# Optimization experiments

Hardware: AMD Instinct MI355X
Metric: run time of the kernel (lower is better)

## Reference

```python
import jax, jax.numpy as jnp
import numpy as np

HIDDEN_DIM = 128


def setup_inputs() -> dict:
    key = jax.random.key(0)
    ks = jax.random.split(key, 7)
    n_edges, edge_dim, edge_hidden, d = 20000, 16, 128, HIDDEN_DIM
    h_v = jax.random.normal(ks[0], (n_edges, d), dtype=jnp.float32)
    h_w = jax.random.normal(ks[1], (n_edges, d), dtype=jnp.float32)
    edge_features = jax.random.normal(ks[2], (n_edges, edge_dim), dtype=jnp.float32)
    W1 = jax.random.normal(ks[3], (edge_dim, edge_hidden), dtype=jnp.float32) * (1.0 / np.sqrt(edge_dim))
    b1 = jnp.zeros((edge_hidden,), dtype=jnp.float32)
    W2 = jax.random.normal(ks[4], (edge_hidden, d * d), dtype=jnp.float32) * (1.0 / np.sqrt(edge_hidden))
    b2 = jnp.zeros((d * d,), dtype=jnp.float32)
    return {"h_v": h_v, "h_w": h_w, "edge_features": edge_features,
            "W1": W1, "b1": b1, "W2": W2, "b2": b2}


def reference(h_v, h_w, edge_features, W1, b1, W2, b2):
    d = HIDDEN_DIM
    # Edge MLP: edge_dim -> edge_hidden -> d*d
    hidden = jax.nn.relu(edge_features @ W1 + b1)          # (E, edge_hidden)
    A = (hidden @ W2 + b2).reshape(-1, d, d)               # (E, d, d) per-edge matrices
    # Batched matrix-vector product: messages_e = A_e @ h_w_e
    messages = jnp.einsum('eij,ej->ei', A, h_w)            # (E, d)
    return messages
```

## Files before the change

kernel.cpp:

```cpp
#include <hip/hip_runtime.h>

#define E_EDGES 20000
#define D_DIM   128
#define NPAIRS  65
#define HSLICES 132

#define NBA 130
#define NBH 313
#define NBC 320

typedef __bf16 bf16x8 __attribute__((ext_vector_type(8)));
typedef float  floatx4 __attribute__((ext_vector_type(4)));

__device__ __forceinline__ unsigned short f32_to_bf16_rne(float f) {
    unsigned int u = __float_as_uint(f);
    unsigned int r = u + 0x7FFFu + ((u >> 16) & 1u);
    return (unsigned short)(r >> 16);
}

__device__ __forceinline__ void gload_lds16(const void* g, void* l) {
    __builtin_amdgcn_global_load_lds(
        (const __attribute__((address_space(1))) unsigned int*)g,
        (__attribute__((address_space(3))) unsigned int*)l, 16, 0, 0);
}

__global__ __launch_bounds__(256) void prep_all(
    const float* __restrict__ W2, const float* __restrict__ b2,
    const float* __restrict__ ef, const float* __restrict__ W1,
    const float* __restrict__ b1, const float* __restrict__ hw,
    uint4* __restrict__ bpf, unsigned int* __restrict__ hTp,
    unsigned short* __restrict__ hwb)
{
    __shared__ __align__(16) char pmem[34816];
    const int bx = blockIdx.x;
    const int t  = threadIdx.x;

    if (bx < NBA) {
        const int h = bx;
        if (h < 129) {
            unsigned short* tile = (unsigned short*)pmem;
            const float* src = (h < 128) ? (W2 + (size_t)h * (D_DIM * D_DIM)) : b2;
            #pragma unroll
            for (int r = 0; r < 16; ++r) {
                const float4 v = ((const float4*)src)[r * 256 + t];
                int c   = (r * 256 + t) * 4;
                int col = c >> 7;
                int k   = c & 127;
                unsigned int u0 = f32_to_bf16_rne(v.x) | ((unsigned int)f32_to_bf16_rne(v.y) << 16);
                unsigned int u1 = f32_to_bf16_rne(v.z) | ((unsigned int)f32_to_bf16_rne(v.w) << 16);
                *(uint2*)&tile[col * 136 + k] = make_uint2(u0, u1);
            }
            __syncthreads();
            #pragma unroll
            for (int r2 = 0; r2 < 8; ++r2) {
                int cidx = r2 * 256 + t;
                int g  = cidx >> 8;
                int s  = (cidx >> 6) & 3;
                int ll = cidx & 63;
                int col = 16 * g + (ll & 15);
                int k0  = 32 * s + 8 * (ll >> 4);
                bpf[(size_t)h * 2048 + cidx] = *(const uint4*)&tile[col * 136 + k0];
            }
        } else {
            #pragma unroll
            for (int r2 = 0; r2 < 8; ++r2)
                bpf[(size_t)h * 2048 + r2 * 256 + t] = make_uint4(0, 0, 0, 0);
        }
    } else if (bx < NBA + NBH) {
        float (*lds_ef)[17] = (float(*)[17])pmem;
        const int b  = bx - NBA;
        const int e0 = b * 64;
        {
            int e  = t >> 2;
            int k4 = (t & 3) * 4;
            int ge = e0 + e;
            float4 v = make_float4(0.f, 0.f, 0.f, 0.f);
            if (ge < E_EDGES) v = *(const float4*)(ef + (size_t)ge * 16 + k4);
            lds_ef[e][k4 + 0] = v.x; lds_ef[e][k4 + 1] = v.y;
            lds_ef[e][k4 + 2] = v.z; lds_ef[e][k4 + 3] = v.w;
        }
        __syncthreads();
        const int e  = t & 63;
        const int hg = t >> 6;
        const bool valid = (e0 + e) < E_EDGES;
        float efr[16];
        #pragma unroll
        for (int k = 0; k < 16; ++k) efr[k] = lds_ef[e][k];
        #pragma unroll 4
        for (int hi2 = 0; hi2 < 16; ++hi2) {
            int h0 = hg * 32 + 2 * hi2;
            float a0 = b1[h0], a1 = b1[h0 + 1];
            #pragma unroll
            for (int k = 0; k < 16; ++k) {
                a0 += efr[k] * W1[k * 128 + h0];
                a1 += efr[k] * W1[k * 128 + h0 + 1];
            }
            unsigned int pk = (unsigned int)f32_to_bf16_rne(fmaxf(a0, 0.f))
                            | ((unsigned int)f32_to_bf16_rne(fmaxf(a1, 0.f)) << 16);
            if (valid) hTp[(size_t)(hg * 16 + hi2) * E_EDGES + e0 + e] = pk;
        }
        if (hg == 0 && valid)
            hTp[(size_t)64 * E_EDGES + e0 + e] = 0x00003F80u;
    } else {
        int i0 = (bx - NBA - NBH) * 256 + t;
        for (int i = i0; i < (E_EDGES * D_DIM) / 4; i += NBC * 256) {
            const float4 v = ((const float4*)hw)[i];
            union { unsigned short u16[4]; uint2 u2; } o;
            o.u16[0] = f32_to_bf16_rne(v.x);
            o.u16[1] = f32_to_bf16_rne(v.y);
            o.u16[2] = f32_to_bf16_rne(v.z);
            o.u16[3] = f32_to_bf16_rne(v.w);
            ((uint2*)hwb)[i] = o.u2;
        }
    }
}

__global__ __launch_bounds__(512, 2)
void edge_main(const uint4* __restrict__ bpf, const unsigned int* __restrict__ hTp,
               const uint4* __restrict__ hwb, float* __restrict__ out) {
    __shared__ __align__(16) char smem[65536];
    const int bx  = blockIdx.x;
    const int ch  = bx & 1;
    const int eg  = bx >> 1;
    const int tid = threadIdx.x;
    const int w   = tid >> 6;
    const int l   = tid & 63;
    const int l4  = l >> 4;
    const int lm  = l & 15;
    const int g   = w & 3;
    const int eh  = w >> 2;
    const int e0  = eg * 160;
    const int eA  = e0 + eh * 80;

    bf16x8 A[5][4];
    #pragma unroll
    for (int m = 0; m < 5; ++m)
        #pragma unroll
        for (int s = 0; s < 4; ++s)
            A[m][s] = ((const bf16x8*)hwb)[(eA + 16 * m + lm) * 16 + 4 * s + l4];

    floatx4 C[5];
    #pragma unroll
    for (int m = 0; m < 5; ++m) C[m] = (floatx4){0.f, 0.f, 0.f, 0.f};
    const floatx4 Zf = (floatx4){0.f, 0.f, 0.f, 0.f};

    const char* bpf_c = (const char*)bpf;

    auto stage = [&](int pair, int p) {
        #pragma unroll
        for (int hh = 0; hh < 2; ++hh) {
            const int h = 2 * pair + hh;
            const char* src = bpf_c + ((size_t)(h * 8 + 4 * ch) * 256) * 16;
            char* dst = smem + p * 32768 + hh * 16384;
            #pragma unroll
            for (int r = 0; r < 2; ++r) {
                const int off = (r * 512 + w * 64) * 16;
                gload_lds16(src + off + l * 16, dst + off);
            }
        }
    };
    auto loadHP = [&](int pair, uint4 (&hp)[5]) {
        const unsigned int* row = hTp + (size_t)pair * E_EDGES + eA + 4 * l4;
        #pragma unroll
        for (int m = 0; m < 5; ++m) hp[m] = *(const uint4*)(row + 16 * m);
    };
    auto computeH = [&](int p, int hh, const uint4 (&hp)[5], bool odd) {
        const bf16x8* Bb = (const bf16x8*)(smem + p * 32768 + hh * 16384) + g * 256 + l;
        bf16x8 B[4];
        #pragma unroll
        for (int s = 0; s < 4; ++s) B[s] = Bb[s * 64];
        #pragma unroll
        for (int m = 0; m < 5; ++m) {
            floatx4 D = __builtin_amdgcn_mfma_f32_16x16x32_bf16(A[m][0], B[0], Zf, 0, 0, 0);
            #pragma unroll
            for (int s = 1; s < 4; ++s)
                D = __builtin_amdgcn_mfma_f32_16x16x32_bf16(A[m][s], B[s], D, 0, 0, 0);
            #pragma unroll
            for (int r = 0; r < 4; ++r) {
                unsigned int u = hp[m][r];
                float sc = odd ? __uint_as_float(u & 0xFFFF0000u)
                               : __uint_as_float(u << 16);
                C[m][r] += sc * D[r];
            }
        }
    };

    uint4 hpa[5], hpb[5];
    stage(0, 0);
    loadHP(0, hpa);
    for (int pr = 0; pr < 64; pr += 2) {
        __syncthreads();
        stage(pr + 1, 1);
        loadHP(pr + 1, hpb);
        computeH(0, 0, hpa, false);
        computeH(0, 1, hpa, true);
        __syncthreads();
        stage(pr + 2, 0);
        loadHP(pr + 2, hpa);
        computeH(1, 0, hpb, false);
        computeH(1, 1, hpb, true);
    }
    __syncthreads();
    computeH(0, 0, hpa, false);
    computeH(0, 1, hpa, true);

    #pragma unroll
    for (int m = 0; m < 5; ++m)
        #pragma unroll
        for (int r = 0; r < 4; ++r)
            out[(size_t)(eA + 16 * m + 4 * l4 + r) * D_DIM + 64 * ch + 16 * g + lm] = C[m][r];
}

extern "C" void kernel_launch(void* const* d_in, const int* in_sizes, int n_in,
                              void* d_out, int out_size, void* d_ws, size_t ws_size,
                              hipStream_t stream) {
    const float* h_w = (const float*)d_in[1];
    const float* ef  = (const float*)d_in[2];
    const float* W1  = (const float*)d_in[3];
    const float* b1  = (const float*)d_in[4];
    const float* W2  = (const float*)d_in[5];
    const float* b2  = (const float*)d_in[6];
    float* out = (float*)d_out;

    char* ws = (char*)d_ws;
    uint4*          bpf = (uint4*)ws;
    unsigned int*   hTp = (unsigned int*)(ws + 4325376);
    unsigned short* hwb = (unsigned short*)(ws + 4325376 + 5200000);

    hipLaunchKernelGGL(prep_all, dim3(NBA + NBH + NBC), dim3(256), 0, stream,
                       W2, b2, ef, W1, b1, h_w, bpf, hTp, hwb);
    hipLaunchKernelGGL(edge_main, dim3(250), dim3(512), 0, stream,
                       bpf, hTp, (const uint4*)hwb, out);
}
```

Measured before the change: 185.4 us.

## Split-K edge_main across two block halves with atomic accumulation into zeroed output

Splits the K (hidden-vector) dimension of the per-edge matvec across two blocks, so each block runs half the MFMAs per slice. Grid size roughly doubles, and the slices are processed four at a time per pipeline stage. Results are merged with atomicAdd into an output cleared by hipMemsetAsync, and launch bounds are raised to request more waves per SIMD. The bpf layout and slice padding (66 pairs) are reworked to match. In exchange it adds an extra memset, atomic traffic, and twice the hTp scale loads across blocks.

```diff
diff --git a/kernel.cpp b/kernel.cpp
--- a/kernel.cpp
+++ b/kernel.cpp
@@ -2,10 +2,10 @@
 
 #define E_EDGES 20000
 #define D_DIM   128
-#define NPAIRS  65
 #define HSLICES 132
-
-#define NBA 130
+#define NPAIRS  66
+
+#define NBA 132
 #define NBH 313
 #define NBC 320
 
@@ -54,11 +54,13 @@
             #pragma unroll
             for (int r2 = 0; r2 < 8; ++r2) {
                 int cidx = r2 * 256 + t;
-                int g  = cidx >> 8;
-                int s  = (cidx >> 6) & 3;
                 int ll = cidx & 63;
-                int col = 16 * g + (ll & 15);
-                int k0  = 32 * s + 8 * (ll >> 4);
+                int sp = (cidx >> 6) & 1;
+                int gp = (cidx >> 7) & 3;
+                int ks = (cidx >> 9) & 1;
+                int ch = (cidx >> 10) & 1;
+                int col = 64 * ch + 16 * gp + (ll & 15);
+                int k0  = 64 * ks + 32 * sp + 8 * (ll >> 4);
                 bpf[(size_t)h * 2048 + cidx] = *(const uint4*)&tile[col * 136 + k0];
             }
         } else {
@@ -88,7 +90,7 @@
         for (int k = 0; k < 16; ++k) efr[k] = lds_ef[e][k];
         #pragma unroll 4
         for (int hi2 = 0; hi2 < 16; ++hi2) {
-            int h0 = hg * 32 + 2 * hi2;
+            const int h0 = __builtin_amdgcn_readfirstlane(hg * 32 + 2 * hi2);
             float a0 = b1[h0], a1 = b1[h0 + 1];
             #pragma unroll
             for (int k = 0; k < 16; ++k) {
@@ -99,8 +101,10 @@
                             | ((unsigned int)f32_to_bf16_rne(fmaxf(a1, 0.f)) << 16);
             if (valid) hTp[(size_t)(hg * 16 + hi2) * E_EDGES + e0 + e] = pk;
         }
-        if (hg == 0 && valid)
+        if (hg == 0 && valid) {
             hTp[(size_t)64 * E_EDGES + e0 + e] = 0x00003F80u;
+            hTp[(size_t)65 * E_EDGES + e0 + e] = 0u;
+        }
     } else {
         int i0 = (bx - NBA - NBH) * 256 + t;
         for (int i = i0; i < (E_EDGES * D_DIM) / 4; i += NBC * 256) {
@@ -115,13 +119,15 @@
     }
 }
 
-__global__ __launch_bounds__(512, 2)
+__global__ __launch_bounds__(512, 4)
 void edge_main(const uint4* __restrict__ bpf, const unsigned int* __restrict__ hTp,
                const uint4* __restrict__ hwb, float* __restrict__ out) {
     __shared__ __align__(16) char smem[65536];
     const int bx  = blockIdx.x;
-    const int ch  = bx & 1;
-    const int eg  = bx >> 1;
+    const int ch  = (bx >> 2) & 1;
+    const int ks  = bx & 1;
+    const int eg  = (bx >> 3) * 2 + ((bx >> 1) & 1);
+    if (eg >= 125) return;
     const int tid = threadIdx.x;
     const int w   = tid >> 6;
     const int l   = tid & 63;
@@ -132,12 +138,12 @@
     const int e0  = eg * 160;
     const int eA  = e0 + eh * 80;
 
-    bf16x8 A[5][4];
+    bf16x8 A[5][2];
     #pragma unroll
     for (int m = 0; m < 5; ++m)
         #pragma unroll
-        for (int s = 0; s < 4; ++s)
-            A[m][s] = ((const bf16x8*)hwb)[(eA + 16 * m + lm) * 16 + 4 * s + l4];
+        for (int sp = 0; sp < 2; ++sp)
+            A[m][sp] = ((const bf16x8*)hwb)[(eA + 16 * m + lm) * 16 + 8 * ks + 4 * sp + l4];
 
     floatx4 C[5];
     #pragma unroll
@@ -146,35 +152,36 @@
 
     const char* bpf_c = (const char*)bpf;
 
-    auto stage = [&](int pair, int p) {
-        #pragma unroll
-        for (int hh = 0; hh < 2; ++hh) {
-            const int h = 2 * pair + hh;
-            const char* src = bpf_c + ((size_t)(h * 8 + 4 * ch) * 256) * 16;
-            char* dst = smem + p * 32768 + hh * 16384;
-            #pragma unroll
-            for (int r = 0; r < 2; ++r) {
-                const int off = (r * 512 + w * 64) * 16;
-                gload_lds16(src + off + l * 16, dst + off);
-            }
+    auto stage = [&](int q, int p) {
+        #pragma unroll
+        for (int r = 0; r < 4; ++r) {
+            const int flat = w * 4 + r;
+            const int hh   = flat >> 3;
+            const int off  = (flat & 7) * 1024;
+            const char* src = bpf_c + (size_t)(4 * q + hh) * 32768
+                            + ch * 16384 + ks * 8192 + off;
+            char* dst = smem + p * 32768 + hh * 8192 + off;
+            gload_lds16(src + l * 16, dst);
         }
     };
-    auto loadHP = [&](int pair, uint4 (&hp)[5]) {
-        const unsigned int* row = hTp + (size_t)pair * E_EDGES + eA + 4 * l4;
-        #pragma unroll
-        for (int m = 0; m < 5; ++m) hp[m] = *(const uint4*)(row + 16 * m);
+    auto loadHP2 = [&](int q, uint4 (&hq)[2][5]) {
+        #pragma unroll
+        for (int pp = 0; pp < 2; ++pp) {
+            const unsigned int* row = hTp + (size_t)(2 * q + pp) * E_EDGES + eA + 4 * l4;
+            #pragma unroll
+            for (int m = 0; m < 5; ++m) hq[pp][m] = *(const uint4*)(row + 16 * m);
+        }
     };
     auto computeH = [&](int p, int hh, const uint4 (&hp)[5], bool odd) {
-        const bf16x8* Bb = (const bf16x8*)(smem + p * 32768 + hh * 16384) + g * 256 + l;
-        bf16x8 B[4];
-        #pragma unroll
-        for (int s = 0; s < 4; ++s) B[s] = Bb[s * 64];
+        const char* slice = smem + p * 32768 + hh * 8192;
+        bf16x8 B[2];
+        #pragma unroll
+        for (int sp = 0; sp < 2; ++sp)
+            B[sp] = *(const bf16x8*)(slice + (g * 2 + sp) * 1024 + l * 16);
         #pragma unroll
         for (int m = 0; m < 5; ++m) {
             floatx4 D = __builtin_amdgcn_mfma_f32_16x16x32_bf16(A[m][0], B[0], Zf, 0, 0, 0);
-            #pragma unroll
-            for (int s = 1; s < 4; ++s)
-                D = __builtin_amdgcn_mfma_f32_16x16x32_bf16(A[m][s], B[s], D, 0, 0, 0);
+            D = __builtin_amdgcn_mfma_f32_16x16x32_bf16(A[m][1], B[1], D, 0, 0, 0);
             #pragma unroll
             for (int r = 0; r < 4; ++r) {
                 unsigned int u = hp[m][r];
@@ -185,30 +192,25 @@
         }
     };
 
-    uint4 hpa[5], hpb[5];
+    uint4 hq[2][5];
     stage(0, 0);
-    loadHP(0, hpa);
-    for (int pr = 0; pr < 64; pr += 2) {
+    for (int q = 0; q < 33; ++q) {
         __syncthreads();
-        stage(pr + 1, 1);
-        loadHP(pr + 1, hpb);
-        computeH(0, 0, hpa, false);
-        computeH(0, 1, hpa, true);
-        __syncthreads();
-        stage(pr + 2, 0);
-        loadHP(pr + 2, hpa);
-        computeH(1, 0, hpb, false);
-        computeH(1, 1, hpb, true);
+        if (q < 32) stage(q + 1, (q + 1) & 1);
+        loadHP2(q, hq);
+        const int p = q & 1;
+        computeH(p, 0, hq[0], false);
+        computeH(p, 1, hq[0], true);
+        computeH(p, 2, hq[1], false);
+        computeH(p, 3, hq[1], true);
     }
-    __syncthreads();
-    computeH(0, 0, hpa, false);
-    computeH(0, 1, hpa, true);
 
     #pragma unroll
     for (int m = 0; m < 5; ++m)
         #pragma unroll
         for (int r = 0; r < 4; ++r)
-            out[(size_t)(eA + 16 * m + 4 * l4 + r) * D_DIM + 64 * ch + 16 * g + lm] = C[m][r];
+            atomicAdd(&out[(size_t)(eA + 16 * m + 4 * l4 + r) * D_DIM
+                           + 64 * ch + 16 * g + lm], C[m][r]);
 }
 
 extern "C" void kernel_launch(void* const* d_in, const int* in_sizes, int n_in,
@@ -225,10 +227,11 @@
     char* ws = (char*)d_ws;
     uint4*          bpf = (uint4*)ws;
     unsigned int*   hTp = (unsigned int*)(ws + 4325376);
-    unsigned short* hwb = (unsigned short*)(ws + 4325376 + 5200000);
+    unsigned short* hwb = (unsigned short*)(ws + 4325376 + 5280000);
 
     hipLaunchKernelGGL(prep_all, dim3(NBA + NBH + NBC), dim3(256), 0, stream,
                        W2, b2, ef, W1, b1, h_w, bpf, hTp, hwb);
-    hipLaunchKernelGGL(edge_main, dim3(250), dim3(512), 0, stream,
+    hipMemsetAsync(out, 0, (size_t)out_size * sizeof(float), stream);
+    hipLaunchKernelGGL(edge_main, dim3(504), dim3(512), 0, stream,
                        bpf, hTp, (const uint4*)hwb, out);
 }
```

Result: slower. 517.6 us (+179.2%).
